# Performance work log

Hardware: AMD Instinct MI355X
Metric: run time of the kernel (lower is better)

The kernel has to match this reference:

```python
import jax, jax.numpy as jnp
import numpy as np

EPS = 1e-6  # torch F.rms_norm uses dtype eps; 1e-6 is the fp32-scale equivalent
ROPE_BASE = 10000.0


def rms_norm(x):
    return x * jax.lax.rsqrt(jnp.mean(x * x, axis=-1, keepdims=True) + EPS)


def rope_tables(T, head_dim, dtype):
    half = head_dim // 2
    t = jnp.arange(T, dtype=jnp.float32)
    inv_freq = 1.0 / (ROPE_BASE ** (jnp.arange(0, head_dim, 2, dtype=jnp.float32) / head_dim))
    freqs = jnp.outer(t, inv_freq)  # [T, half]
    return jnp.cos(freqs).astype(dtype), jnp.sin(freqs).astype(dtype)


def apply_rotary(x, cos, sin):
    # x: [B, T, H, D]; cos/sin: [T, D//2]
    d = x.shape[-1] // 2
    x1, x2 = x[..., :d], x[..., d:]
    c = cos[None, :, None, :]
    s = sin[None, :, None, :]
    return jnp.concatenate([x1 * c + x2 * s, -x1 * s + x2 * c], axis=-1)


def setup_inputs() -> dict:
    key = jax.random.key(0)
    ks = jax.random.split(key, 8)
    B, T, E, H, D = 4, 2048, 768, 6, 128
    std = 0.5 * E ** (-0.5)
    bound = (3.0 ** 0.5) * std
    u = lambda k, shp: jax.random.uniform(k, shp, jnp.float32, -bound, bound)
    return {
        "x": jax.random.normal(ks[0], (B, T, E), jnp.float32),
        "v1": jax.random.normal(ks[1], (B, T, 1, D), jnp.float32),
        "Wq": u(ks[2], (E, E)),
        "Wk": u(ks[3], (D, E)),
        "Wv": u(ks[4], (D, E)),
        "lamb": jnp.float32(0.5),
        "Wo": jax.random.normal(ks[5], (E, E), jnp.float32) * 0.02,
        "Wg": jax.random.normal(ks[6], (H, 12), jnp.float32) * 0.02,
    }


def reference(x, v1, Wq, Wk, Wv, lamb, Wo, Wg):
    B, T, E = x.shape
    H, D = 6, E // 6
    attn_scale = 0.1

    q = (x @ Wq.T).reshape(B, T, H, D)          # [B,T,H,D]
    k = (x @ Wk.T).reshape(B, T, 1, D)          # [B,T,1,D]
    v = (x @ Wv.T).reshape(B, T, 1, D)

    # value residual lambda-mix (v1 already has head_dim -> no val_proj)
    v = (1.0 - lamb) * v + lamb * v1            # [B,T,1,D]

    q, k = rms_norm(q), rms_norm(k)
    cos, sin = rope_tables(T, D, x.dtype)
    q = apply_rotary(q, cos, sin)
    k = apply_rotary(k, cos, sin)

    k1 = k[:, :, 0, :]                          # [B,T,D] single KV head (GQA)
    v1h = v[:, :, 0, :]

    scores = jnp.einsum('bthd,bsd->bhts', q, k1) * attn_scale
    causal = jnp.tril(jnp.ones((T, T), dtype=bool))
    scores = jnp.where(causal[None, None], scores, jnp.finfo(scores.dtype).min)
    probs = jax.nn.softmax(scores, axis=-1)
    y = jnp.einsum('bhts,bsd->bthd', probs, v1h)  # [B,T,H,D]

    gate = jax.nn.sigmoid(x[..., :Wg.shape[-1]] @ Wg.T)  # [B,T,H]
    y = y * gate[..., None]
    y = y.reshape(B, T, E)
    return (y @ Wo.T, v1)
```

## Files before the change

kernel.cpp:

```cpp
#include <hip/hip_runtime.h>
#include <hip/hip_bf16.h>
#include <math.h>

#define B_ 4
#define T_ 2048
#define E_ 768
#define H_ 6
#define D_ 128
#define M_ (B_*T_)

typedef __attribute__((ext_vector_type(8))) short short8;
typedef __attribute__((ext_vector_type(4))) float f32x4;
typedef __attribute__((ext_vector_type(4))) unsigned int u32x4;
typedef unsigned short u16;
typedef unsigned int u32;

__device__ inline u16 f2b(float x) {
  union { float f; unsigned u; } c; c.f = x;
  unsigned r = (c.u + 0x7fff + ((c.u >> 16) & 1)) >> 16;
  return (u16)r;
}
__device__ inline float b2f(u16 x) {
  union { unsigned u; float f; } c; c.u = ((unsigned)x) << 16;
  return c.f;
}
__device__ inline u32 pkbf(float a, float b) {
  union { float f; u32 u; } ca, cb; ca.f = a; cb.f = b;
  return ((ca.u + 0x8000u) >> 16) | ((cb.u + 0x8000u) & 0xffff0000u);
}

__global__ void k_rope_tables(float* __restrict__ cosT, float* __restrict__ sinT) {
  int t = blockIdx.x;
  int j = threadIdx.x;
  float inv = powf(10000.0f, -(float)j * (1.0f/64.0f));
  float f = (float)t * inv;
  cosT[t*64 + j] = cosf(f);
  sinT[t*64 + j] = sinf(f);
}

template<int ABF16>
__global__ __launch_bounds__(256) void k_gemm(
    const void* __restrict__ Ap, const float* __restrict__ W0,
    const float* __restrict__ W1, const float* __restrict__ W2,
    int nyq, void* __restrict__ Cout, int ldc, int outBf16) {
  __shared__ __align__(16) u16 As[128*64];
  __shared__ __align__(16) u16 Bs[128*64];
  const int tid  = threadIdx.x;
  const int lane = tid & 63;
  const int wv   = tid >> 6;
  const int lo   = lane & 15;
  const int hi   = lane >> 4;
  const int wm   = wv >> 1;
  const int wn   = wv & 1;
  const int m0   = blockIdx.x * 128;
  const int by   = blockIdx.y;

  const float* W; int wr0, cb;
  if (by < nyq)       { W = W0; wr0 = by*128; cb = by*128; }
  else if (by == nyq) { W = W1; wr0 = 0;      cb = nyq*128; }
  else                { W = W2; wr0 = 0;      cb = nyq*128 + 128; }

  f32x4 acc[4][4];
  #pragma unroll
  for (int i = 0; i < 4; ++i)
    #pragma unroll
    for (int j = 0; j < 4; ++j) {
      acc[i][j][0]=0.f; acc[i][j][1]=0.f; acc[i][j][2]=0.f; acc[i][j][3]=0.f;
    }

  for (int k0 = 0; k0 < E_; k0 += 64) {
    __syncthreads();
    #pragma unroll
    for (int i = 0; i < 4; ++i) {
      int s   = i*256 + tid;
      int row = s >> 3;
      int sl  = s & 7;
      int ba  = (row*128 + sl*16) ^ ((row & 7) << 4);
      if (ABF16) {
        short8 va = *reinterpret_cast<const short8*>(
            (const u16*)Ap + (size_t)(m0+row)*E_ + k0 + sl*8);
        *(short8*)((char*)As + ba) = va;
      } else {
        const float* af = (const float*)Ap + (size_t)(m0+row)*E_ + k0 + sl*8;
        float4 f0 = *reinterpret_cast<const float4*>(af);
        float4 f1 = *reinterpret_cast<const float4*>(af + 4);
        u32x4 pk;
        pk[0]=pkbf(f0.x,f0.y); pk[1]=pkbf(f0.z,f0.w);
        pk[2]=pkbf(f1.x,f1.y); pk[3]=pkbf(f1.z,f1.w);
        *(u32x4*)((char*)As + ba) = pk;
      }
      {
        const float* wf = W + (size_t)(wr0+row)*E_ + k0 + sl*8;
        float4 f0 = *reinterpret_cast<const float4*>(wf);
        float4 f1 = *reinterpret_cast<const float4*>(wf + 4);
        u32x4 pk;
        pk[0]=pkbf(f0.x,f0.y); pk[1]=pkbf(f0.z,f0.w);
        pk[2]=pkbf(f1.x,f1.y); pk[3]=pkbf(f1.z,f1.w);
        *(u32x4*)((char*)Bs + ba) = pk;
      }
    }
    __syncthreads();
    #pragma unroll
    for (int ks = 0; ks < 2; ++ks) {
      short8 af[4], bf[4];
      #pragma unroll
      for (int mi = 0; mi < 4; ++mi) {
        int row = wm*64 + mi*16 + lo;
        int ba = (row*128 + ks*64 + hi*16) ^ ((row & 7) << 4);
        af[mi] = *(const short8*)((char*)As + ba);
      }
      #pragma unroll
      for (int nf = 0; nf < 4; ++nf) {
        int row = wn*64 + nf*16 + lo;
        int ba = (row*128 + ks*64 + hi*16) ^ ((row & 7) << 4);
        bf[nf] = *(const short8*)((char*)Bs + ba);
      }
      #pragma unroll
      for (int mi = 0; mi < 4; ++mi)
        #pragma unroll
        for (int nf = 0; nf < 4; ++nf)
          acc[mi][nf] = __builtin_amdgcn_mfma_f32_16x16x32_bf16(
              af[mi], bf[nf], acc[mi][nf], 0, 0, 0);
    }
  }

  #pragma unroll
  for (int mi = 0; mi < 4; ++mi)
    #pragma unroll
    for (int nf = 0; nf < 4; ++nf)
      #pragma unroll
      for (int r = 0; r < 4; ++r) {
        int m = m0 + wm*64 + mi*16 + hi*4 + r;
        int n = cb + wn*64 + nf*16 + lo;
        float v = acc[mi][nf][r];
        if (outBf16) ((u16*)Cout)[(size_t)m*ldc + n] = f2b(v);
        else         ((float*)Cout)[(size_t)m*ldc + n] = v;
      }
}

__global__ __launch_bounds__(128) void k_vmix_norm_rope(
    const u16* __restrict__ qkv, const float* __restrict__ v1,
    const float* __restrict__ lambp,
    const float* __restrict__ cosT, const float* __restrict__ sinT,
    u16* __restrict__ qn, u16* __restrict__ kn, u16* __restrict__ vn) {
  const int bt  = blockIdx.x;
  const int row = blockIdx.y;
  const int d   = threadIdx.x;
  const int t   = bt & (T_-1);
  const int b   = bt >> 11;
  float val = b2f(qkv[(size_t)bt*1024 + row*128 + d]);
  if (row == 7) {
    float lamb = *lambp;
    float mix = (1.0f - lamb)*val + lamb*v1[(size_t)bt*128 + d];
    vn[(size_t)bt*128 + d] = f2b(mix);
    return;
  }
  __shared__ float red[2];
  __shared__ float nbuf[128];
  float ss = val*val;
  #pragma unroll
  for (int off = 32; off > 0; off >>= 1) ss += __shfl_xor(ss, off);
  if ((threadIdx.x & 63) == 0) red[threadIdx.x >> 6] = ss;
  __syncthreads();
  float sum = red[0] + red[1];
  float r = rsqrtf(sum * (1.0f/128.0f) + 1e-6f);
  nbuf[d] = val * r;
  __syncthreads();
  int j = d & 63;
  float c = cosT[t*64 + j];
  float s = sinT[t*64 + j];
  float o = (d < 64) ? (nbuf[d]*c + nbuf[d+64]*s)
                     : (-nbuf[d-64]*s + nbuf[d]*c);
  if (row < 6) qn[((size_t)(b*H_ + row)*T_ + t)*D_ + d] = f2b(o);
  else         kn[(size_t)bt*D_ + d] = f2b(o);
}

__global__ __launch_bounds__(256) void k_transpose_v(
    const u16* __restrict__ vn, u16* __restrict__ vnt) {
  __shared__ u16 tile[64][136];
  const int tid = threadIdx.x;
  const int b  = blockIdx.y;
  const int t0 = blockIdx.x * 64;
  {
    int tr = tid >> 2;
    int dc = (tid & 3) * 32;
    const u16* src = vn + ((size_t)(b*T_ + t0 + tr))*D_ + dc;
    #pragma unroll
    for (int j = 0; j < 4; ++j) {
      short8 v = *reinterpret_cast<const short8*>(src + j*8);
      *reinterpret_cast<short8*>(&tile[tr][dc + j*8]) = v;
    }
  }
  __syncthreads();
  {
    int dr = tid >> 1;
    int tc = (tid & 1) * 32;
    #pragma unroll
    for (int j = 0; j < 4; ++j) {
      short8 o;
      #pragma unroll
      for (int jj = 0; jj < 8; ++jj) o[jj] = (short)tile[tc + j*8 + jj][dr];
      *reinterpret_cast<short8*>(
          vnt + ((size_t)(b*D_ + dr))*T_ + t0 + tc + j*8) = o;
    }
  }
}

#define KVB 32
__global__ __launch_bounds__(256) void k_attn_mfma(
    const u16* __restrict__ qn, const u16* __restrict__ kn,
    const u16* __restrict__ vnt, const float* __restrict__ x,
    const float* __restrict__ Wg, u16* __restrict__ yb) {
  __shared__ __align__(16) u16 Pl[4*1024];
  __shared__ u32   Pacc[3][32][64];
  __shared__ float Lacc[3][32];

  const int tid  = threadIdx.x;
  const int lane = tid & 63;
  const int wv   = tid >> 6;
  const int lo   = lane & 15;
  const int hi   = lane >> 4;

  const int bid  = blockIdx.x;
  const int rank = bid / 24;
  const int bh   = bid % 24;
  const int h    = bh % H_;
  const int b    = bh / H_;
  const int t0w  = (63 - rank) * 32;

  short8 qa[2][4];
  const u16* qb = qn + ((size_t)(b*H_ + h)*T_ + t0w)*D_;
  #pragma unroll
  for (int qi = 0; qi < 2; ++qi)
    #pragma unroll
    for (int ks = 0; ks < 4; ++ks)
      qa[qi][ks] = *(const short8*)(qb + (size_t)(qi*16 + lo)*D_ + ks*32 + hi*8);

  f32x4 acc[2][8];
  float lrow[2][4];
  #pragma unroll
  for (int qi = 0; qi < 2; ++qi) {
    #pragma unroll
    for (int dj = 0; dj < 8; ++dj) {
      acc[qi][dj][0]=0.f; acc[qi][dj][1]=0.f; acc[qi][dj][2]=0.f; acc[qi][dj][3]=0.f;
    }
    #pragma unroll
    for (int r = 0; r < 4; ++r) lrow[qi][r] = 0.f;
  }

  const u16* kg  = kn  + (size_t)b*T_*D_;
  const u16* vgt = vnt + (size_t)b*D_*T_;

  int kv0 = wv*KVB;
  if (kv0 <= t0w) {
    short8 kb[2][4];
    #pragma unroll
    for (int kj = 0; kj < 2; ++kj)
      #pragma unroll
      for (int ks = 0; ks < 4; ++ks)
        kb[kj][ks] = *(const short8*)(
            kg + (size_t)(kv0 + kj*16 + lo)*D_ + ks*32 + hi*8);

    #pragma unroll 2
    for (; kv0 <= t0w; kv0 += 4*KVB) {
      const int kvn = kv0 + 4*KVB;
      const bool more = (kvn <= t0w);
      short8 kbn[2][4];
      if (more) {
        #pragma unroll
        for (int kj = 0; kj < 2; ++kj)
          #pragma unroll
          for (int ks = 0; ks < 4; ++ks)
            kbn[kj][ks] = *(const short8*)(
                kg + (size_t)(kvn + kj*16 + lo)*D_ + ks*32 + hi*8);
      }
      short8 vb[8];
      #pragma unroll
      for (int dj = 0; dj < 8; ++dj)
        vb[dj] = *(const short8*)(
            vgt + (size_t)(dj*16 + lo)*T_ + kv0 + hi*8);

      f32x4 sc[2][2];
      #pragma unroll
      for (int qi = 0; qi < 2; ++qi)
        #pragma unroll
        for (int kj = 0; kj < 2; ++kj) {
          sc[qi][kj][0]=0.f; sc[qi][kj][1]=0.f; sc[qi][kj][2]=0.f; sc[qi][kj][3]=0.f;
        }
      #pragma unroll
      for (int kj = 0; kj < 2; ++kj)
        #pragma unroll
        for (int qi = 0; qi < 2; ++qi)
          #pragma unroll
          for (int ks = 0; ks < 4; ++ks)
            sc[qi][kj] = __builtin_amdgcn_mfma_f32_16x16x32_bf16(
                qa[qi][ks], kb[kj][ks], sc[qi][kj], 0, 0, 0);

      const bool dm = (kv0 == t0w);
      float p[2][2][4];
      #pragma unroll
      for (int qi = 0; qi < 2; ++qi) {
        #pragma unroll
        for (int r = 0; r < 4; ++r) {
          float p0 = __expf(fmaf(sc[qi][0][r], 0.1f, -12.8f));
          float p1 = __expf(fmaf(sc[qi][1][r], 0.1f, -12.8f));
          if (dm) {
            int row = t0w + qi*16 + hi*4 + r;
            p0 = (kv0 + lo      <= row) ? p0 : 0.f;
            p1 = (kv0 + 16 + lo <= row) ? p1 : 0.f;
          }
          lrow[qi][r] += p0 + p1;
          p[qi][0][r] = p0; p[qi][1][r] = p1;
        }
      }

      #pragma unroll
      for (int qi = 0; qi < 2; ++qi)
        #pragma unroll
        for (int kj = 0; kj < 2; ++kj)
          #pragma unroll
          for (int r = 0; r < 4; ++r) {
            int row = qi*16 + hi*4 + r;
            int col = kj*16 + lo;
            int ba = (row*64 + col*2) ^ ((row & 7) << 4);
            *(u16*)((char*)Pl + wv*2048 + ba) = f2b(p[qi][kj][r]);
          }
      short8 pa[2];
      #pragma unroll
      for (int qi = 0; qi < 2; ++qi) {
        int row = qi*16 + lo;
        int ba = (row*64 + hi*16) ^ ((row & 7) << 4);
        pa[qi] = *(const short8*)((char*)Pl + wv*2048 + ba);
      }
      #pragma unroll
      for (int dj = 0; dj < 8; ++dj)
        #pragma unroll
        for (int qi = 0; qi < 2; ++qi)
          acc[qi][dj] = __builtin_amdgcn_mfma_f32_16x16x32_bf16(
              pa[qi], vb[dj], acc[qi][dj], 0, 0, 0);

      if (more) {
        #pragma unroll
        for (int kj = 0; kj < 2; ++kj)
          #pragma unroll
          for (int ks = 0; ks < 4; ++ks)
            kb[kj][ks] = kbn[kj][ks];
      }
    }
  }

  #pragma unroll
  for (int qi = 0; qi < 2; ++qi)
    #pragma unroll
    for (int r = 0; r < 4; ++r) {
      float lv = lrow[qi][r];
      lv += __shfl_xor(lv, 1);
      lv += __shfl_xor(lv, 2);
      lv += __shfl_xor(lv, 4);
      lv += __shfl_xor(lv, 8);
      lrow[qi][r] = lv;
    }

  if (wv > 0) {
    #pragma unroll
    for (int qi = 0; qi < 2; ++qi) {
      #pragma unroll
      for (int dj = 0; dj < 8; ++dj)
        #pragma unroll
        for (int rp = 0; rp < 2; ++rp) {
          u32 pk = (u32)f2b(acc[qi][dj][2*rp]) |
                   ((u32)f2b(acc[qi][dj][2*rp+1]) << 16);
          Pacc[wv-1][(qi*8 + dj)*2 + rp][lane] = pk;
        }
      #pragma unroll
      for (int r = 0; r < 4; ++r)
        if (lo == 0) Lacc[wv-1][(qi*4 + r)*4 + hi] = lrow[qi][r];
    }
  }
  __syncthreads();
  if (wv > 0) return;

  #pragma unroll
  for (int qi = 0; qi < 2; ++qi) {
    #pragma unroll
    for (int dj = 0; dj < 8; ++dj)
      #pragma unroll
      for (int rp = 0; rp < 2; ++rp) {
        #pragma unroll
        for (int w = 0; w < 3; ++w) {
          u32 pk = Pacc[w][(qi*8 + dj)*2 + rp][lane];
          acc[qi][dj][2*rp]   += b2f((u16)(pk & 0xffff));
          acc[qi][dj][2*rp+1] += b2f((u16)(pk >> 16));
        }
      }
    #pragma unroll
    for (int r = 0; r < 4; ++r)
      #pragma unroll
      for (int w = 0; w < 3; ++w)
        lrow[qi][r] += Lacc[w][(qi*4 + r)*4 + hi];
  }

  #pragma unroll
  for (int qi = 0; qi < 2; ++qi)
    #pragma unroll
    for (int r = 0; r < 4; ++r) {
      int trow = t0w + qi*16 + hi*4 + r;
      size_t bt = (size_t)b*T_ + trow;
      float dotg = 0.f;
      #pragma unroll
      for (int jj = 0; jj < 12; ++jj)
        dotg += x[bt*E_ + jj]*Wg[h*12 + jj];
      float g = 1.f/(1.f + __expf(-dotg));
      float coef = g / lrow[qi][r];
      #pragma unroll
      for (int dj = 0; dj < 8; ++dj)
        yb[bt*E_ + h*D_ + dj*16 + lo] = f2b(acc[qi][dj][r]*coef);
    }
}

extern "C" void kernel_launch(void* const* d_in, const int* in_sizes, int n_in,
                              void* d_out, int out_size, void* d_ws, size_t ws_size,
                              hipStream_t stream) {
  const float* x    = (const float*)d_in[0];
  const float* v1   = (const float*)d_in[1];
  const float* Wq   = (const float*)d_in[2];
  const float* Wk   = (const float*)d_in[3];
  const float* Wv   = (const float*)d_in[4];
  const float* lamb = (const float*)d_in[5];
  const float* Wo   = (const float*)d_in[6];
  const float* Wg   = (const float*)d_in[7];
  float* out = (float*)d_out;

  u16* qkvb = (u16*)d_ws;
  u16* qn   = qkvb + (size_t)M_*1024;
  u16* kn   = qn   + (size_t)M_*E_;
  u16* vn   = kn   + (size_t)M_*D_;
  u16* vnt  = vn   + (size_t)M_*D_;
  u16* yb   = vnt  + (size_t)M_*D_;
  float* cosT = (float*)(yb + (size_t)M_*E_);
  float* sinT = cosT + T_*64;

  k_rope_tables<<<T_, 64, 0, stream>>>(cosT, sinT);

  k_gemm<0><<<dim3(M_/128, 8), 256, 0, stream>>>(
      x, Wq, Wk, Wv, 6, qkvb, 1024, 1);

  k_vmix_norm_rope<<<dim3(M_, 8), 128, 0, stream>>>(qkvb, v1, lamb, cosT, sinT,
                                                    qn, kn, vn);
  k_transpose_v<<<dim3(T_/64, B_), 256, 0, stream>>>(vn, vnt);

  k_attn_mfma<<<B_*H_*(T_/32), 256, 0, stream>>>(qn, kn, vnt, x, Wg, yb);

  k_gemm<1><<<dim3(M_/128, 6), 256, 0, stream>>>(
      yb, Wo, Wo, Wo, 6, out, 768, 0);

  hipMemcpyAsync(out + (size_t)M_*E_, v1, (size_t)M_*D_*sizeof(float),
                 hipMemcpyDeviceToDevice, stream);
}
```

Measured before the change: 276.0 us.

## Pre-pack K and V into MFMA fragment order for coalesced attention loads

Replaces the V transpose kernel with a packing kernel that rearranges both K and V into the exact per-lane MFMA operand layout, 512 elements per 16x32 fragment. The attention kernel then loads each fragment as one contiguous 1 KB read per wave, with lane*8 offsets, instead of strided row reads. This is meant to cut scattered global and L2 traffic in the attention inner loop. The cost is one extra packed K buffer and a slightly heavier pre-pass.

```diff
diff --git a/kernel.cpp b/kernel.cpp
--- a/kernel.cpp
+++ b/kernel.cpp
@@ -175,41 +175,50 @@
   else         kn[(size_t)bt*D_ + d] = f2b(o);
 }
 
-__global__ __launch_bounds__(256) void k_transpose_v(
-    const u16* __restrict__ vn, u16* __restrict__ vnt) {
-  __shared__ u16 tile[64][136];
+__global__ __launch_bounds__(256) void k_pack_frags(
+    const u16* __restrict__ kn, const u16* __restrict__ vn,
+    u16* __restrict__ kf, u16* __restrict__ vf) {
+  __shared__ u16 Lk[32][136];
+  __shared__ u16 Lv[32][136];
   const int tid = threadIdx.x;
-  const int b  = blockIdx.y;
-  const int t0 = blockIdx.x * 64;
+  const int g = blockIdx.x;
+  const int b = blockIdx.y;
+  const int t0 = g*32;
   {
-    int tr = tid >> 2;
-    int dc = (tid & 3) * 32;
-    const u16* src = vn + ((size_t)(b*T_ + t0 + tr))*D_ + dc;
-    #pragma unroll
-    for (int j = 0; j < 4; ++j) {
-      short8 v = *reinterpret_cast<const short8*>(src + j*8);
-      *reinterpret_cast<short8*>(&tile[tr][dc + j*8]) = v;
-    }
+    int r = tid >> 3, c = (tid & 7)*16;
+    const u16* ksrc = kn + ((size_t)(b*T_) + t0 + r)*D_ + c;
+    const u16* vsrc = vn + ((size_t)(b*T_) + t0 + r)*D_ + c;
+    *(short8*)&Lk[r][c]   = *(const short8*)ksrc;
+    *(short8*)&Lk[r][c+8] = *(const short8*)(ksrc+8);
+    *(short8*)&Lv[r][c]   = *(const short8*)vsrc;
+    *(short8*)&Lv[r][c+8] = *(const short8*)(vsrc+8);
   }
   __syncthreads();
-  {
-    int dr = tid >> 1;
-    int tc = (tid & 1) * 32;
-    #pragma unroll
-    for (int j = 0; j < 4; ++j) {
-      short8 o;
-      #pragma unroll
-      for (int jj = 0; jj < 8; ++jj) o[jj] = (short)tile[tc + j*8 + jj][dr];
-      *reinterpret_cast<short8*>(
-          vnt + ((size_t)(b*D_ + dr))*T_ + t0 + tc + j*8) = o;
-    }
+  const int lane = tid & 63, wv = tid >> 6;
+  const int lo = lane & 15, hi = lane >> 4;
+  #pragma unroll
+  for (int it = 0; it < 2; ++it) {
+    int kt = wv >> 1;
+    int ks = (wv & 1) + it*2;
+    short8 v = *(const short8*)&Lk[kt*16 + lo][ks*32 + hi*8];
+    size_t base = ((((size_t)b*128) + g*2 + kt)*4 + ks)*512;
+    *(short8*)(kf + base + lane*8) = v;
+  }
+  #pragma unroll
+  for (int it = 0; it < 2; ++it) {
+    int dj = wv + it*4;
+    short8 o;
+    #pragma unroll
+    for (int j = 0; j < 8; ++j) o[j] = (short)Lv[hi*8 + j][dj*16 + lo];
+    size_t base = (((size_t)b*64 + g)*8 + dj)*512;
+    *(short8*)(vf + base + lane*8) = o;
   }
 }
 
 #define KVB 32
 __global__ __launch_bounds__(256) void k_attn_mfma(
-    const u16* __restrict__ qn, const u16* __restrict__ kn,
-    const u16* __restrict__ vnt, const float* __restrict__ x,
+    const u16* __restrict__ qn, const u16* __restrict__ kf,
+    const u16* __restrict__ vf, const float* __restrict__ x,
     const float* __restrict__ Wg, u16* __restrict__ yb) {
   __shared__ __align__(16) u16 Pl[4*1024];
   __shared__ u32   Pacc[3][32][64];
@@ -248,8 +257,8 @@
     for (int r = 0; r < 4; ++r) lrow[qi][r] = 0.f;
   }
 
-  const u16* kg  = kn  + (size_t)b*T_*D_;
-  const u16* vgt = vnt + (size_t)b*D_*T_;
+  const u16* kfb = kf + (size_t)b*128*4*512;
+  const u16* vfb = vf + (size_t)b*64*8*512;
 
   int kv0 = wv*KVB;
   if (kv0 <= t0w) {
@@ -259,7 +268,7 @@
       #pragma unroll
       for (int ks = 0; ks < 4; ++ks)
         kb[kj][ks] = *(const short8*)(
-            kg + (size_t)(kv0 + kj*16 + lo)*D_ + ks*32 + hi*8);
+            kfb + (size_t)(((kv0>>4) + kj)*4 + ks)*512 + lane*8);
 
     #pragma unroll 2
     for (; kv0 <= t0w; kv0 += 4*KVB) {
@@ -272,13 +281,13 @@
           #pragma unroll
           for (int ks = 0; ks < 4; ++ks)
             kbn[kj][ks] = *(const short8*)(
-                kg + (size_t)(kvn + kj*16 + lo)*D_ + ks*32 + hi*8);
+                kfb + (size_t)(((kvn>>4) + kj)*4 + ks)*512 + lane*8);
       }
       short8 vb[8];
       #pragma unroll
       for (int dj = 0; dj < 8; ++dj)
         vb[dj] = *(const short8*)(
-            vgt + (size_t)(dj*16 + lo)*T_ + kv0 + hi*8);
+            vfb + (size_t)((kv0>>5)*8 + dj)*512 + lane*8);
 
       f32x4 sc[2][2];
       #pragma unroll
@@ -435,8 +444,9 @@
   u16* qn   = qkvb + (size_t)M_*1024;
   u16* kn   = qn   + (size_t)M_*E_;
   u16* vn   = kn   + (size_t)M_*D_;
-  u16* vnt  = vn   + (size_t)M_*D_;
-  u16* yb   = vnt  + (size_t)M_*D_;
+  u16* kfr  = vn   + (size_t)M_*D_;
+  u16* vfr  = kfr  + (size_t)M_*D_;
+  u16* yb   = vfr  + (size_t)M_*D_;
   float* cosT = (float*)(yb + (size_t)M_*E_);
   float* sinT = cosT + T_*64;
 
@@ -447,9 +457,9 @@
 
   k_vmix_norm_rope<<<dim3(M_, 8), 128, 0, stream>>>(qkvb, v1, lamb, cosT, sinT,
                                                     qn, kn, vn);
-  k_transpose_v<<<dim3(T_/64, B_), 256, 0, stream>>>(vn, vnt);
-
-  k_attn_mfma<<<B_*H_*(T_/32), 256, 0, stream>>>(qn, kn, vnt, x, Wg, yb);
+  k_pack_frags<<<dim3(T_/32, B_), 256, 0, stream>>>(kn, vn, kfr, vfr);
+
+  k_attn_mfma<<<B_*H_*(T_/32), 256, 0, stream>>>(qn, kfr, vfr, x, Wg, yb);
 
   k_gemm<1><<<dim3(M_/128, 6), 256, 0, stream>>>(
       yb, Wo, Wo, Wo, 6, out, 768, 0);
```

New measurement: 226.4 us. -18.0%, faster.
